# Optimization experiments

Hardware: AMD Instinct MI355X
Metric: run time of the kernel (lower is better)

The kernel has to match this reference:

```python
import math
import jax, jax.numpy as jnp
import numpy as np

NUM_HEADS = 8
HEAD_DIM = 64


def setup_inputs() -> dict:
    key = jax.random.key(0)
    k1, k2, k3, k4 = jax.random.split(key, 4)
    C = 256
    E = NUM_HEADS * HEAD_DIM  # 512
    x = jax.random.normal(k1, (4, C, 48, 48), dtype=jnp.float32)
    Wqkv = jax.random.normal(k2, (3 * E, C), dtype=jnp.float32) * (1.0 / math.sqrt(C))
    Wout = jax.random.normal(k3, (C, E), dtype=jnp.float32) * (1.0 / math.sqrt(E))
    bout = jax.random.normal(k4, (C,), dtype=jnp.float32) * 0.01
    return {"x": x, "Wqkv": Wqkv, "Wout": Wout, "bout": bout}


def reference(x, Wqkv, Wout, bout):
    b, c, H, W = x.shape
    nh, hd = NUM_HEADS, HEAD_DIM
    N = H * W
    scale = 1.0 / math.sqrt(hd)
    # 1x1 conv (no bias) == channel matmul
    qkv = jnp.einsum('bcxy,oc->boxy', x, Wqkv)            # [b, 3*nh*hd, H, W]
    qkv = qkv.reshape(b, 3, nh, hd, N)                    # channel split order: (k, h, d)
    q, k, v = qkv[:, 0], qkv[:, 1], qkv[:, 2]             # each [b, nh, hd, N]
    att = jnp.einsum('bhdi,bhdj->bhij', q, k) * scale     # [b, nh, N, N]
    att = jax.nn.softmax(att, axis=-1)                    # stable (max-subtract inside)
    out = jnp.einsum('bhij,bhdj->bhid', att, v)           # [b, nh, N, hd]
    out = out.transpose(0, 1, 3, 2).reshape(b, nh * hd, H, W)  # 'b h (x y) d -> b (h d) x y'
    # 1x1 conv with bias
    return jnp.einsum('bexy,ce->bcxy', out, Wout) + bout[None, :, None, None]
```

## Files before the change

kernel.cpp:

```cpp
#include <hip/hip_runtime.h>

typedef __attribute__((ext_vector_type(8))) __bf16 bf16x8;
typedef __attribute__((ext_vector_type(16))) float f32x16;
typedef __attribute__((ext_vector_type(4))) float f32x4;
typedef __attribute__((ext_vector_type(4))) unsigned short us4;

__device__ __forceinline__ unsigned short f2bf(float f) {
  __bf16 h = (__bf16)f;
  return __builtin_bit_cast(unsigned short, h);
}
__device__ __forceinline__ unsigned pack2bf(float lo, float hi) {
  return (unsigned)f2bf(lo) | ((unsigned)f2bf(hi) << 16);
}

__device__ __forceinline__ void stage_chunks(const unsigned short* g, int ld,
                                             unsigned short* lds, int rows, int tid) {
  int total = rows * 8;
  for (int c0 = 0; c0 < total; c0 += 256) {
    int c = c0 + tid;
    int row = c >> 3, kc = c & 7;
    const unsigned short* src = g + (size_t)row * ld + ((kc ^ (row & 7)) << 3);
    unsigned short* dst = lds + (size_t)(c0 + (tid & 192)) * 8;
    __builtin_amdgcn_global_load_lds((const __attribute__((address_space(1))) void*)src,
                                     (__attribute__((address_space(3))) void*)dst,
                                     16, 0, 0);
  }
}

__device__ __forceinline__ bf16x8 frag(const unsigned short* lds, int row, int kc) {
  return *(const bf16x8*)(lds + row * 64 + ((kc ^ (row & 7)) << 3));
}


__global__ void k_cvt(const float* __restrict__ in, unsigned short* __restrict__ outp, int n) {
  int i = (blockIdx.x * 256 + threadIdx.x) * 4;
  if (i + 3 < n) {
    f32x4 v = *(const f32x4*)(in + i);
    us4 o;
#pragma unroll
    for (int k = 0; k < 4; k++) o[k] = f2bf(v[k]);
    *(us4*)(outp + i) = o;
  }
}

__global__ __launch_bounds__(256) void k_xpose(const float* __restrict__ x,
                                               unsigned short* __restrict__ xT) {
  __shared__ float t[32][33];
  int tid = threadIdx.x;
  int col = tid & 31, rowb = tid >> 5;
  int nt = blockIdx.x * 32, ct = blockIdx.y * 32, b = blockIdx.z;
  const float* src = x + ((size_t)b * 256 + ct) * 2304 + nt;
#pragma unroll
  for (int rr = 0; rr < 32; rr += 8) t[rowb + rr][col] = src[(size_t)(rowb + rr) * 2304 + col];
  __syncthreads();
  unsigned short* dst = xT + ((size_t)b * 2304 + nt) * 256 + ct;
#pragma unroll
  for (int rr = 0; rr < 32; rr += 8) dst[(size_t)(rowb + rr) * 256 + col] = f2bf(t[col][rowb + rr]);
}

__global__ __launch_bounds__(256, 2) void k_gemm_qkv(
    const unsigned short* __restrict__ W, const unsigned short* __restrict__ xT,
    unsigned short* __restrict__ qT, unsigned short* __restrict__ kT,
    unsigned short* __restrict__ vv) {
  __shared__ unsigned short As[128 * 64];
  __shared__ unsigned short Bs[128 * 64];
  int tid = threadIdx.x, lane = tid & 63, wid = tid >> 6;
  int m0 = blockIdx.x * 128, n0 = blockIdx.y * 128, b = blockIdx.z;
  const unsigned short* Ag = W + (size_t)m0 * 256;
  const unsigned short* Bg = xT + ((size_t)b * 2304 + n0) * 256;
  int wm = (wid >> 1) * 64, wn = (wid & 1) * 64;
  f32x4 acc[4][4] = {};
  for (int kt = 0; kt < 256; kt += 64) {
    __syncthreads();
    stage_chunks(Ag + kt, 256, As, 128, tid);
    stage_chunks(Bg + kt, 256, Bs, 128, tid);
    __syncthreads();
#pragma unroll
    for (int kk = 0; kk < 2; kk++) {
      bf16x8 af[4], bf[4];
#pragma unroll
      for (int i = 0; i < 4; i++) af[i] = frag(As, wm + i * 16 + (lane & 15), kk * 4 + (lane >> 4));
#pragma unroll
      for (int j = 0; j < 4; j++) bf[j] = frag(Bs, wn + j * 16 + (lane & 15), kk * 4 + (lane >> 4));
#pragma unroll
      for (int i = 0; i < 4; i++)
#pragma unroll
        for (int j = 0; j < 4; j++)
          acc[i][j] = __builtin_amdgcn_mfma_f32_16x16x32_bf16(af[i], bf[j], acc[i][j], 0, 0, 0);
    }
  }
#pragma unroll
  for (int i = 0; i < 4; i++) {
    int o = m0 + wm + i * 16 + ((lane >> 4) << 2);
    int which = o >> 9, h = (o >> 6) & 7, d0 = o & 63;
#pragma unroll
    for (int j = 0; j < 4; j++) {
      int n = n0 + wn + j * 16 + (lane & 15);
      if (which == 2) {
#pragma unroll
        for (int jj = 0; jj < 4; jj++)
          vv[((size_t)(b * 8 + h) * 64 + d0 + jj) * 2304 + n] = f2bf(acc[i][j][jj]);
      } else {
        float sc = which ? 1.0f : 0.18033688011112042f;
        us4 pk;
#pragma unroll
        for (int jj = 0; jj < 4; jj++) pk[jj] = f2bf(acc[i][j][jj] * sc);
        unsigned short* dst = (which ? kT : qT) + ((size_t)(b * 8 + h) * 2304 + n) * 64 + d0;
        *(us4*)dst = pk;
      }
    }
  }
}

__global__ __launch_bounds__(256, 3) void k_attn(
    const unsigned short* __restrict__ qT, const unsigned short* __restrict__ kT,
    const unsigned short* __restrict__ vv, unsigned short* __restrict__ o2T) {
  __shared__ unsigned short Qs[128 * 64];
  __shared__ unsigned short Ks[2][64 * 64];
  __shared__ unsigned short Vs[2][64 * 64];
  int tid = threadIdx.x, lane = tid & 63, wid = tid >> 6;
  int il = lane & 31, g = lane >> 5;
  int i0 = blockIdx.x * 128, bh = blockIdx.y;
  stage_chunks(qT + ((size_t)bh * 2304 + i0) * 64, 64, Qs, 128, tid);
  stage_chunks(kT + (size_t)bh * 2304 * 64, 64, Ks[0], 64, tid);
  stage_chunks(vv + (size_t)bh * 64 * 2304, 2304, Vs[0], 64, tid);
  __syncthreads();
  bf16x8 qf[4];
#pragma unroll
  for (int ks = 0; ks < 4; ks++) qf[ks] = frag(Qs, wid * 32 + il, ks * 2 + g);
  float mrun = -1e30f, lrun = 0.f;
  f32x16 O0 = {}, O1 = {};
  for (int t = 0; t < 36; t++) {
    const unsigned short* Kc = Ks[t & 1];
    const unsigned short* Vc = Vs[t & 1];
    if (t + 1 < 36) {
      stage_chunks(kT + ((size_t)bh * 2304 + (t + 1) * 64) * 64, 64, Ks[(t + 1) & 1], 64, tid);
      stage_chunks(vv + (size_t)bh * 64 * 2304 + (t + 1) * 64, 2304, Vs[(t + 1) & 1], 64, tid);
    }
    f32x16 S0 = {}, S1 = {};
#pragma unroll
    for (int ks = 0; ks < 4; ks++) {
      bf16x8 kf0 = frag(Kc, il, ks * 2 + g);
      bf16x8 kf1 = frag(Kc, 32 + il, ks * 2 + g);
      S0 = __builtin_amdgcn_mfma_f32_32x32x16_bf16(kf0, qf[ks], S0, 0, 0, 0);
      S1 = __builtin_amdgcn_mfma_f32_32x32x16_bf16(kf1, qf[ks], S1, 0, 0, 0);
    }
    float pm = -1e30f;
#pragma unroll
    for (int r = 0; r < 16; r++) pm = fmaxf(pm, fmaxf(S0[r], S1[r]));
    pm = fmaxf(pm, __shfl_xor(pm, 32));
    float nm = fmaxf(mrun, pm);
    float al = __builtin_amdgcn_exp2f(mrun - nm);
    mrun = nm;
    float rs = 0.f;
#pragma unroll
    for (int r = 0; r < 16; r++) {
      S0[r] = __builtin_amdgcn_exp2f(S0[r] - nm);
      S1[r] = __builtin_amdgcn_exp2f(S1[r] - nm);
      rs += S0[r] + S1[r];
    }
    rs += __shfl_xor(rs, 32);
    lrun = lrun * al + rs;
#pragma unroll
    for (int r = 0; r < 16; r++) { O0[r] *= al; O1[r] *= al; }
    unsigned w0[8], w1[8];
#pragma unroll
    for (int m = 0; m < 8; m++) {
      w0[m] = pack2bf(S0[2 * m], S0[2 * m + 1]);
      w1[m] = pack2bf(S1[2 * m], S1[2 * m + 1]);
    }
#pragma unroll
    for (int ks = 0; ks < 4; ks++) {
      int a = ks & 1;
      unsigned A0, A1, B0, B1;
      if (ks >> 1) { A0 = w1[4 * a]; A1 = w1[4 * a + 1]; B0 = w1[4 * a + 2]; B1 = w1[4 * a + 3]; }
      else         { A0 = w0[4 * a]; A1 = w0[4 * a + 1]; B0 = w0[4 * a + 2]; B1 = w0[4 * a + 3]; }
      unsigned send0 = g ? A0 : B0, send1 = g ? A1 : B1;
      unsigned pw0 = __shfl_xor(send0, 32), pw1 = __shfl_xor(send1, 32);
      union { unsigned u[4]; bf16x8 v; } F;
      F.u[0] = g ? pw0 : A0;
      F.u[1] = g ? pw1 : A1;
      F.u[2] = g ? B0 : pw0;
      F.u[3] = g ? B1 : pw1;
      bf16x8 vf0 = frag(Vc, il, ks * 2 + g);
      bf16x8 vf1 = frag(Vc, 32 + il, ks * 2 + g);
      O0 = __builtin_amdgcn_mfma_f32_32x32x16_bf16(vf0, F.v, O0, 0, 0, 0);
      O1 = __builtin_amdgcn_mfma_f32_32x32x16_bf16(vf1, F.v, O1, 0, 0, 0);
    }
    __syncthreads();
  }
  float rl = 1.0f / lrun;
  int b = bh >> 3, h = bh & 7;
  unsigned short* dst = o2T + ((size_t)b * 2304 + (i0 + wid * 32 + il)) * 512 + h * 64;
#pragma unroll
  for (int dt = 0; dt < 2; dt++) {
#pragma unroll
    for (int u = 0; u < 4; u++) {
      us4 pk;
#pragma unroll
      for (int v = 0; v < 4; v++) {
        float val = (dt ? O1[4 * u + v] : O0[4 * u + v]) * rl;
        pk[v] = f2bf(val);
      }
      *(us4*)(dst + dt * 32 + 8 * u + 4 * g) = pk;
    }
  }
}

__global__ __launch_bounds__(256, 2) void k_gemm_out(
    const unsigned short* __restrict__ Wo, const unsigned short* __restrict__ o2T,
    const float* __restrict__ bout, float* __restrict__ out) {
  __shared__ unsigned short As[128 * 64];
  __shared__ unsigned short Bs[128 * 64];
  int tid = threadIdx.x, lane = tid & 63, wid = tid >> 6;
  int m0 = blockIdx.x * 128, n0 = blockIdx.y * 128, b = blockIdx.z;
  const unsigned short* Ag = Wo + (size_t)m0 * 512;
  const unsigned short* Bg = o2T + ((size_t)b * 2304 + n0) * 512;
  int wm = (wid >> 1) * 64, wn = (wid & 1) * 64;
  f32x4 acc[4][4] = {};
  for (int kt = 0; kt < 512; kt += 64) {
    __syncthreads();
    stage_chunks(Ag + kt, 512, As, 128, tid);
    stage_chunks(Bg + kt, 512, Bs, 128, tid);
    __syncthreads();
#pragma unroll
    for (int kk = 0; kk < 2; kk++) {
      bf16x8 af[4], bf[4];
#pragma unroll
      for (int i = 0; i < 4; i++) af[i] = frag(As, wm + i * 16 + (lane & 15), kk * 4 + (lane >> 4));
#pragma unroll
      for (int j = 0; j < 4; j++) bf[j] = frag(Bs, wn + j * 16 + (lane & 15), kk * 4 + (lane >> 4));
#pragma unroll
      for (int i = 0; i < 4; i++)
#pragma unroll
        for (int j = 0; j < 4; j++)
          acc[i][j] = __builtin_amdgcn_mfma_f32_16x16x32_bf16(af[i], bf[j], acc[i][j], 0, 0, 0);
    }
  }
#pragma unroll
  for (int i = 0; i < 4; i++) {
    int c = m0 + wm + i * 16 + ((lane >> 4) << 2);
#pragma unroll
    for (int j = 0; j < 4; j++) {
      int n = n0 + wn + j * 16 + (lane & 15);
#pragma unroll
      for (int jj = 0; jj < 4; jj++)
        out[((size_t)b * 256 + c + jj) * 2304 + n] = acc[i][j][jj] + bout[c + jj];
    }
  }
}

extern "C" void kernel_launch(void* const* d_in, const int* in_sizes, int n_in,
                              void* d_out, int out_size, void* d_ws, size_t ws_size,
                              hipStream_t stream) {
  const float* x = (const float*)d_in[0];
  const float* Wqkv = (const float*)d_in[1];
  const float* Wout = (const float*)d_in[2];
  const float* bout = (const float*)d_in[3];
  float* out = (float*)d_out;
  char* ws = (char*)d_ws;
  unsigned short* Wqkv_bf = (unsigned short*)(ws + 0);
  unsigned short* Wout_bf = (unsigned short*)(ws + 786432);
  unsigned short* xT      = (unsigned short*)(ws + 1048576);
  unsigned short* qT      = (unsigned short*)(ws + 5767168);
  unsigned short* kT      = (unsigned short*)(ws + 15204352);
  unsigned short* vv      = (unsigned short*)(ws + 24641536);
  unsigned short* o2T     = (unsigned short*)(ws + 34078720);

  k_cvt<<<dim3(384), dim3(256), 0, stream>>>(Wqkv, Wqkv_bf, 1536 * 256);
  k_cvt<<<dim3(128), dim3(256), 0, stream>>>(Wout, Wout_bf, 256 * 512);
  k_xpose<<<dim3(72, 8, 4), dim3(256), 0, stream>>>(x, xT);
  k_gemm_qkv<<<dim3(12, 18, 4), dim3(256), 0, stream>>>(Wqkv_bf, xT, qT, kT, vv);
  k_attn<<<dim3(18, 32), dim3(256), 0, stream>>>(qT, kT, vv, o2T);
  k_gemm_out<<<dim3(2, 18, 4), dim3(256), 0, stream>>>(Wout_bf, o2T, bout, out);
}
```

Baseline: 136.1 us.

## Split attention KV range across wave pairs with 64-row query tiles and XCD-aware mapping

```diff
diff --git a/kernel.cpp b/kernel.cpp
--- a/kernel.cpp
+++ b/kernel.cpp
@@ -112,31 +112,35 @@
   }
 }
 
-__global__ __launch_bounds__(256, 3) void k_attn(
+__global__ __launch_bounds__(256, 4) void k_attn(
     const unsigned short* __restrict__ qT, const unsigned short* __restrict__ kT,
     const unsigned short* __restrict__ vv, unsigned short* __restrict__ o2T) {
-  __shared__ unsigned short Qs[128 * 64];
   __shared__ unsigned short Ks[2][64 * 64];
   __shared__ unsigned short Vs[2][64 * 64];
-  int tid = threadIdx.x, lane = tid & 63, wid = tid >> 6;
+  int tid = threadIdx.x, lane = tid & 63;
+  int wid = tid >> 6, rh = wid & 1, jh = wid >> 1;
   int il = lane & 31, g = lane >> 5;
-  int i0 = blockIdx.x * 128, bh = blockIdx.y;
-  stage_chunks(qT + ((size_t)bh * 2304 + i0) * 64, 64, Qs, 128, tid);
-  stage_chunks(kT + (size_t)bh * 2304 * 64, 64, Ks[0], 64, tid);
-  stage_chunks(vv + (size_t)bh * 64 * 2304, 2304, Vs[0], 64, tid);
-  __syncthreads();
+  int lin = blockIdx.x;
+  int xcd = lin & 7, idx = lin >> 3;
+  int bh = xcd * 4 + idx / 36;
+  int i0 = (idx % 36) * 64;
+  const unsigned short* qrow = qT + ((size_t)bh * 2304 + i0 + rh * 32 + il) * 64;
   bf16x8 qf[4];
 #pragma unroll
-  for (int ks = 0; ks < 4; ks++) qf[ks] = frag(Qs, wid * 32 + il, ks * 2 + g);
+  for (int ks = 0; ks < 4; ks++) qf[ks] = *(const bf16x8*)(qrow + (ks * 2 + g) * 8);
   float mrun = -1e30f, lrun = 0.f;
   f32x16 O0 = {}, O1 = {};
-  for (int t = 0; t < 36; t++) {
-    const unsigned short* Kc = Ks[t & 1];
-    const unsigned short* Vc = Vs[t & 1];
-    if (t + 1 < 36) {
-      stage_chunks(kT + ((size_t)bh * 2304 + (t + 1) * 64) * 64, 64, Ks[(t + 1) & 1], 64, tid);
-      stage_chunks(vv + (size_t)bh * 64 * 2304 + (t + 1) * 64, 2304, Vs[(t + 1) & 1], 64, tid);
-    }
+  const size_t kbase = (size_t)bh * 2304 * 64;
+  const size_t vbase = (size_t)bh * 64 * 2304;
+  for (int t = 0; t < 18; t++) {
+    if (t) __syncthreads();
+    stage_chunks(kT + kbase + (size_t)t * 64 * 64, 64, Ks[0], 64, tid);
+    stage_chunks(kT + kbase + (size_t)(18 + t) * 64 * 64, 64, Ks[1], 64, tid);
+    stage_chunks(vv + vbase + t * 64, 2304, Vs[0], 64, tid);
+    stage_chunks(vv + vbase + (18 + t) * 64, 2304, Vs[1], 64, tid);
+    __syncthreads();
+    const unsigned short* Kc = Ks[jh];
+    const unsigned short* Vc = Vs[jh];
     f32x16 S0 = {}, S1 = {};
 #pragma unroll
     for (int ks = 0; ks < 4; ks++) {
@@ -145,24 +149,37 @@
       S0 = __builtin_amdgcn_mfma_f32_32x32x16_bf16(kf0, qf[ks], S0, 0, 0, 0);
       S1 = __builtin_amdgcn_mfma_f32_32x32x16_bf16(kf1, qf[ks], S1, 0, 0, 0);
     }
-    float pm = -1e30f;
-#pragma unroll
-    for (int r = 0; r < 16; r++) pm = fmaxf(pm, fmaxf(S0[r], S1[r]));
-    pm = fmaxf(pm, __shfl_xor(pm, 32));
-    float nm = fmaxf(mrun, pm);
-    float al = __builtin_amdgcn_exp2f(mrun - nm);
-    mrun = nm;
-    float rs = 0.f;
+    float t0[16];
+#pragma unroll
+    for (int r = 0; r < 16; r++) t0[r] = fmaxf(S0[r], S1[r]);
+#pragma unroll
+    for (int s = 8; s >= 1; s >>= 1)
+#pragma unroll
+      for (int r = 0; r < 8; r++)
+        if (r < s) t0[r] = fmaxf(t0[r], t0[r + s]);
+    float pm = fmaxf(t0[0], __shfl_xor(t0[0], 32));
+    if (!__all(pm - mrun <= 8.0f)) {
+      float nm = fmaxf(mrun, pm);
+      float al = __builtin_amdgcn_exp2f(mrun - nm);
+      mrun = nm; lrun *= al;
+#pragma unroll
+      for (int r = 0; r < 16; r++) { O0[r] *= al; O1[r] *= al; }
+    }
 #pragma unroll
     for (int r = 0; r < 16; r++) {
-      S0[r] = __builtin_amdgcn_exp2f(S0[r] - nm);
-      S1[r] = __builtin_amdgcn_exp2f(S1[r] - nm);
-      rs += S0[r] + S1[r];
-    }
-    rs += __shfl_xor(rs, 32);
-    lrun = lrun * al + rs;
-#pragma unroll
-    for (int r = 0; r < 16; r++) { O0[r] *= al; O1[r] *= al; }
+      S0[r] = __builtin_amdgcn_exp2f(S0[r] - mrun);
+      S1[r] = __builtin_amdgcn_exp2f(S1[r] - mrun);
+    }
+    float a16[16];
+#pragma unroll
+    for (int r = 0; r < 16; r++) a16[r] = S0[r] + S1[r];
+#pragma unroll
+    for (int s = 8; s >= 1; s >>= 1)
+#pragma unroll
+      for (int r = 0; r < 8; r++)
+        if (r < s) a16[r] += a16[r + s];
+    float rs = a16[0] + __shfl_xor(a16[0], 32);
+    lrun += rs;
     unsigned w0[8], w1[8];
 #pragma unroll
     for (int m = 0; m < 8; m++) {
@@ -187,22 +204,41 @@
       O0 = __builtin_amdgcn_mfma_f32_32x32x16_bf16(vf0, F.v, O0, 0, 0, 0);
       O1 = __builtin_amdgcn_mfma_f32_32x32x16_bf16(vf1, F.v, O1, 0, 0, 0);
     }
-    __syncthreads();
-  }
-  float rl = 1.0f / lrun;
-  int b = bh >> 3, h = bh & 7;
-  unsigned short* dst = o2T + ((size_t)b * 2304 + (i0 + wid * 32 + il)) * 512 + h * 64;
-#pragma unroll
-  for (int dt = 0; dt < 2; dt++) {
-#pragma unroll
-    for (int u = 0; u < 4; u++) {
-      us4 pk;
-#pragma unroll
-      for (int v = 0; v < 4; v++) {
-        float val = (dt ? O1[4 * u + v] : O0[4 * u + v]) * rl;
-        pk[v] = f2bf(val);
+  }
+  __syncthreads();
+  float* sm = (float*)Ks;
+  float* ml = (float*)Vs;
+  if (jh == 1) {
+#pragma unroll
+    for (int r = 0; r < 16; r++) {
+      sm[(rh * 32 + r) * 64 + lane] = O0[r];
+      sm[(rh * 32 + 16 + r) * 64 + lane] = O1[r];
+    }
+    if (!g) { ml[rh * 64 + il] = mrun; ml[rh * 64 + 32 + il] = lrun; }
+  }
+  __syncthreads();
+  if (jh == 0) {
+    float m1 = ml[rh * 64 + il], l1 = ml[rh * 64 + 32 + il];
+    float m = fmaxf(mrun, m1);
+    float a0 = __builtin_amdgcn_exp2f(mrun - m);
+    float a1 = __builtin_amdgcn_exp2f(m1 - m);
+    float rl = 1.0f / (lrun * a0 + l1 * a1);
+    int b = bh >> 3, h = bh & 7;
+    unsigned short* dst = o2T + ((size_t)b * 2304 + (i0 + rh * 32 + il)) * 512 + h * 64;
+#pragma unroll
+    for (int dt = 0; dt < 2; dt++) {
+#pragma unroll
+      for (int u = 0; u < 4; u++) {
+        us4 pk;
+#pragma unroll
+        for (int v = 0; v < 4; v++) {
+          int r = 4 * u + v;
+          float own = dt ? O1[r] : O0[r];
+          float oth = sm[(rh * 32 + dt * 16 + r) * 64 + lane];
+          pk[v] = f2bf((own * a0 + oth * a1) * rl);
+        }
+        *(us4*)(dst + dt * 32 + 8 * u + 4 * g) = pk;
       }
-      *(us4*)(dst + dt * 32 + 8 * u + 4 * g) = pk;
     }
   }
 }
@@ -271,6 +307,6 @@
   k_cvt<<<dim3(128), dim3(256), 0, stream>>>(Wout, Wout_bf, 256 * 512);
   k_xpose<<<dim3(72, 8, 4), dim3(256), 0, stream>>>(x, xT);
   k_gemm_qkv<<<dim3(12, 18, 4), dim3(256), 0, stream>>>(Wqkv_bf, xT, qT, kT, vv);
-  k_attn<<<dim3(18, 32), dim3(256), 0, stream>>>(qT, kT, vv, o2T);
+  k_attn<<<dim3(1152), dim3(256), 0, stream>>>(qT, kT, vv, o2T);
   k_gemm_out<<<dim3(2, 18, 4), dim3(256), 0, stream>>>(Wout_bf, o2T, bout, out);
 }
```

Result: faster. 123.2 us (-9.5%).
